# Kernel tuning notes

Hardware: AMD Instinct MI355X
Metric: run time of the kernel (lower is better)

## Reference

```python
import jax, jax.numpy as jnp
import numpy as np

NUM_CODES = 1024
EMBED_DIM = 64
COMMITMENT_COST = 0.25
ENTROPY_WEIGHT = 0.1
N_TOKENS = 131072


def setup_inputs() -> dict:
    key = jax.random.key(0)
    k1, k2 = jax.random.split(key)
    z_e = jax.random.normal(k1, (N_TOKENS, EMBED_DIM), dtype=jnp.float32)
    # nn.Embedding init: uniform(-1/num_codes, 1/num_codes)
    codebook = jax.random.uniform(
        k2, (NUM_CODES, EMBED_DIM), dtype=jnp.float32,
        minval=-1.0 / NUM_CODES, maxval=1.0 / NUM_CODES)
    return {"z_e": z_e, "codebook": codebook}


def reference(z_e, codebook):
    # Squared euclidean distances; argmin is invariant to sqrt so skip it.
    # d2[n,k] = |z_n|^2 - 2 z_n.e_k + |e_k|^2
    z_sq = jnp.sum(z_e * z_e, axis=-1, keepdims=True)          # [N,1]
    e_sq = jnp.sum(codebook * codebook, axis=-1)               # [K]
    d2 = z_sq - 2.0 * (z_e @ codebook.T) + e_sq[None, :]       # [N,K]
    indices = jnp.argmin(d2, axis=-1)                          # [N] int

    z_q = codebook[indices]                                    # [N,D] gather

    codebook_loss = jnp.mean((jax.lax.stop_gradient(z_q) - z_e) ** 2)
    commitment_loss = COMMITMENT_COST * jnp.mean(
        (z_q - jax.lax.stop_gradient(z_e)) ** 2)

    # Code-usage histogram via scatter-add (avoids materializing [N,K] one-hot).
    n = z_e.shape[0]
    counts = jnp.zeros((NUM_CODES,), dtype=z_e.dtype).at[indices].add(1.0)
    avg_probs = counts / n + 1e-10
    entropy = -jnp.sum(avg_probs * jnp.log(avg_probs))
    max_entropy = np.log(NUM_CODES)
    entropy_loss = -ENTROPY_WEIGHT * (entropy / max_entropy)
    perplexity = jnp.exp(entropy)

    # Straight-through estimator
    z_q_st = z_e + jax.lax.stop_gradient(z_q - z_e)

    return (z_q_st, indices, codebook_loss, commitment_loss,
            entropy_loss, perplexity)
```

## Files before the change

### kernel.cpp

```cpp
#include <hip/hip_runtime.h>
#include <float.h>
#include <math.h>

#define K_CODES 1024
#define ED 64
#define NTOK 131072
#define EPS 4e-4f

typedef __attribute__((ext_vector_type(8)))  short short8;
typedef __attribute__((ext_vector_type(16))) float float16;


static __device__ __forceinline__ unsigned short f2bf(float x) {
    unsigned u = __float_as_uint(x);
    u += 0x7fffu + ((u >> 16) & 1u);
    return (unsigned short)(u >> 16);
}
static __device__ __forceinline__ float bf2f(unsigned short h) {
    return __uint_as_float(((unsigned)h) << 16);
}

__global__ __launch_bounds__(256) void vq_codes(const float* __restrict__ cb,
                                                float* __restrict__ e_sq,
                                                short8* __restrict__ efH,
                                                short8* __restrict__ efL,
                                                unsigned int* __restrict__ counts,
                                                float* __restrict__ sse_part)
{
#pragma clang fp contract(off)
    const int k = blockIdx.x * 256 + threadIdx.x;
    const float4* ep = (const float4*)(cb + (size_t)k * ED);
    const int m = k & 31, ct = k >> 5;
    float r[8];
#pragma unroll
    for (int g = 0; g < 8; ++g) {
        float4 a = ep[2 * g], b = ep[2 * g + 1];
        float v[8] = {a.x, a.y, a.z, a.w, b.x, b.y, b.z, b.w};
        short8 hv, lv;
#pragma unroll
        for (int j = 0; j < 8; ++j) {
            unsigned short hb = f2bf(v[j]);
            hv[j] = (short)hb;
            lv[j] = (short)f2bf(v[j] - bf2f(hb));
            const float sq = v[j] * v[j];
            r[j] = g ? (r[j] + sq) : sq;
        }
        efH[(ct * 8 + g) * 32 + m] = hv;
        efL[(ct * 8 + g) * 32 + m] = lv;
    }
    e_sq[k] = ((r[0] + r[1]) + (r[2] + r[3])) + ((r[4] + r[5]) + (r[6] + r[7]));
    counts[k]        = 0u;
    counts[k + 1024] = 0u;
    counts[k + 2048] = 0u;
    counts[k + 3072] = 0u;
    if (k < 64) sse_part[k] = 0.f;
}

#define RESCORE(cc)                                                          \
    do {                                                                     \
        const int c_ = (cc);                                                 \
        const float4* e4_ = (const float4*)(cb + (size_t)c_ * ED);           \
        float a_ = 0.f;                                                      \
        _Pragma("unroll")                                                    \
        for (int jj_ = 0; jj_ < 16; ++jj_) {                                 \
            const float4 v_ = e4_[jj_];                                      \
            a_ = fmaf(zr[4 * jj_ + 0], v_.x, a_);                            \
            a_ = fmaf(zr[4 * jj_ + 1], v_.y, a_);                            \
            a_ = fmaf(zr[4 * jj_ + 2], v_.z, a_);                            \
            a_ = fmaf(zr[4 * jj_ + 3], v_.w, a_);                            \
        }                                                                    \
        const float d2_ = fmaf(-2.f, a_, zsq) + e_sq[c_];                    \
        if (d2_ < best || (d2_ == best && c_ < bi)) { best = d2_; bi = c_; } \
    } while (0)

__global__ __launch_bounds__(256, 3) void vq_main(const float* __restrict__ z_e,
                                                  const float* __restrict__ cb,
                                                  const float* __restrict__ e_sq,
                                                  const short8* __restrict__ efH,
                                                  const short8* __restrict__ efL,
                                                  float* __restrict__ out_zq,
                                                  float* __restrict__ out_idx,
                                                  unsigned int* __restrict__ counts,
                                                  float* __restrict__ sse_part)
{
#pragma clang fp contract(off)
    __shared__ short8 s_zfh[512];
    __shared__ short8 s_zfl[512];
    __shared__ float2 s_sel[32 * 64];
    __shared__ int    s_bi[64];
    __shared__ float  s_wsse[4];

    const int tid = threadIdx.x;
    const int wv = tid >> 6, lane = tid & 63;
    const int h = lane >> 5, ml = lane & 31;
    const int t0 = blockIdx.x * 64;

    {
        const float4* zp = (const float4*)(z_e + (size_t)(t0 + lane) * ED);
        const int n = lane & 31, ttl = lane >> 5;
#pragma unroll
        for (int gg = 0; gg < 2; ++gg) {
            const int g = wv * 2 + gg;
            float4 a = zp[2 * g], b = zp[2 * g + 1];
            float v[8] = {a.x, a.y, a.z, a.w, b.x, b.y, b.z, b.w};
            short8 hv, lv;
#pragma unroll
            for (int j = 0; j < 8; ++j) {
                unsigned short hb = f2bf(v[j]);
                hv[j] = (short)hb;
                lv[j] = (short)f2bf(v[j] - bf2f(hb));
            }
            s_zfh[(ttl * 8 + g) * 32 + n] = hv;
            s_zfl[(ttl * 8 + g) * 32 + n] = lv;
        }
    }
    __syncthreads();

#pragma unroll
    for (int g = 0; g < 4; ++g) {
        short8 ea[2][4], eb[2][4];
#pragma unroll
        for (int mt = 0; mt < 2; ++mt) {
            const int ct = g * 8 + wv * 2 + mt;
#pragma unroll
            for (int q = 0; q < 4; ++q) {
                const int idx = (ct * 8 + q * 2 + h) * 32 + ml;
                ea[mt][q] = efH[idx];
                eb[mt][q] = efL[idx];
            }
        }
#pragma unroll
        for (int it = 0; it < 2; ++it) {
            float16 acc0 = {}, acc1 = {};
#pragma unroll
            for (int q = 0; q < 4; ++q) {
                const int idx = (it * 8 + q * 2 + h) * 32 + ml;
                const short8 zh = s_zfh[idx];
                const short8 zl = s_zfl[idx];
                acc0 = __builtin_amdgcn_mfma_f32_32x32x16_bf16(ea[0][q], zh, acc0, 0, 0, 0);
                acc1 = __builtin_amdgcn_mfma_f32_32x32x16_bf16(ea[1][q], zh, acc1, 0, 0, 0);
                acc0 = __builtin_amdgcn_mfma_f32_32x32x16_bf16(ea[0][q], zl, acc0, 0, 0, 0);
                acc1 = __builtin_amdgcn_mfma_f32_32x32x16_bf16(ea[1][q], zl, acc1, 0, 0, 0);
                acc0 = __builtin_amdgcn_mfma_f32_32x32x16_bf16(eb[0][q], zh, acc0, 0, 0, 0);
                acc1 = __builtin_amdgcn_mfma_f32_32x32x16_bf16(eb[1][q], zh, acc1, 0, 0, 0);
            }
#pragma unroll
            for (int mt = 0; mt < 2; ++mt) {
                const float16 acc = mt ? acc1 : acc0;
                float tv1[8], tv2[8];
                int   ti[8];
#pragma unroll
                for (int p = 0; p < 8; ++p) {
                    const float a = acc[2 * p], b = acc[2 * p + 1];
                    const int ia = ((2 * p) & 3) + 8 * ((2 * p) >> 2) + 4 * h;
                    const int ib = ((2 * p + 1) & 3) + 8 * ((2 * p + 1) >> 2) + 4 * h;
                    const bool gt = b > a;
                    tv1[p] = gt ? b : a;
                    ti[p]  = gt ? ib : ia;
                    tv2[p] = gt ? a : b;
                }
#pragma unroll
                for (int s = 4; s >= 1; s >>= 1) {
#pragma unroll
                    for (int p = 0; p < s; ++p) {
                        const float av1 = tv1[2 * p], bv1 = tv1[2 * p + 1];
                        const bool gt = bv1 > av1;
                        const float inner = gt ? av1 : bv1;
                        tv1[p] = gt ? bv1 : av1;
                        ti[p]  = gt ? ti[2 * p + 1] : ti[2 * p];
                        tv2[p] = fmaxf(fmaxf(tv2[2 * p], tv2[2 * p + 1]), inner);
                    }
                }
                float v1 = tv1[0], v2 = tv2[0];
                int i1 = ti[0];
                const float o1 = __shfl_xor(v1, 32);
                const float o2 = __shfl_xor(v2, 32);
                const int   oi = __shfl_xor(i1, 32);
                const float lo = fminf(v1, o1);
                if (o1 > v1) { v1 = o1; i1 = oi; }
                v2 = fmaxf(lo, fmaxf(v2, o2));
                if (lane < 32) {
                    const unsigned bits = (__float_as_uint(-2.f * v1) & ~31u) | (unsigned)i1;
                    float2 o;
                    o.x = __uint_as_float(bits);
                    o.y = -2.f * v2;
                    s_sel[(g * 8 + wv * 2 + mt) * 64 + it * 32 + lane] = o;
                }
            }
        }
    }
    __syncthreads();

    if (wv < 2) {
        const int tls = (wv & 1) * 32 + ml;
        const int t = t0 + tls;
        float av[16], bv[16];
        float m = FLT_MAX;
#pragma unroll
        for (int i = 0; i < 16; ++i) {
            const float2 p = s_sel[(h * 16 + i) * 64 + tls];
            av[i] = p.x; bv[i] = p.y;
            m = fminf(m, av[i]);
        }
        m = fminf(m, __shfl_xor(m, 32));
        const float thr = m + EPS;

        unsigned band16 = 0u, full16 = 0u;
        int cand0 = 0, nb = 0;
#pragma unroll
        for (int i = 0; i < 16; ++i) {
            if (av[i] <= thr) {
                if (nb == 0)
                    cand0 = (h * 16 + i) * 32 + (int)(__float_as_uint(av[i]) & 31u);
                ++nb;
                band16 |= (1u << i);
                if (bv[i] <= thr) full16 |= (1u << i);
            }
        }
        const int nb_o = __shfl_xor(nb, 32);
        const int c0_o = __shfl_xor(cand0, 32);
        const unsigned full_o = (unsigned)__shfl_xor((int)full16, 32);

        int bsel;
        if ((nb + nb_o) == 1 && (full16 | full_o) == 0u) {
            bsel = h == 0 ? (nb ? cand0 : c0_o) : (nb_o ? c0_o : cand0);
        } else {
            const float4* zp = (const float4*)(z_e + (size_t)t * ED);
            float zr[ED];
#pragma unroll
            for (int i = 0; i < 16; ++i) {
                const float4 v = zp[i];
                zr[4 * i + 0] = v.x; zr[4 * i + 1] = v.y;
                zr[4 * i + 2] = v.z; zr[4 * i + 3] = v.w;
            }
            float r[8];
#pragma unroll
            for (int g2 = 0; g2 < 8; ++g2) {
#pragma unroll
                for (int j = 0; j < 8; ++j) {
                    const float sq = zr[g2 * 8 + j] * zr[g2 * 8 + j];
                    r[j] = g2 ? (r[j] + sq) : sq;
                }
            }
            const float zsq = ((r[0] + r[1]) + (r[2] + r[3])) + ((r[4] + r[5]) + (r[6] + r[7]));
            float best = FLT_MAX;
            int bi = 0;
            unsigned rem = band16;
            while (rem) {
                const int i = __ffs(rem) - 1;
                rem &= rem - 1;
                const int ct = h * 16 + i;
                if (full16 & (1u << i)) {
                    for (int j = 0; j < 32; ++j) RESCORE(ct * 32 + j);
                } else {
                    RESCORE(ct * 32 + (int)(__float_as_uint(av[i]) & 31u));
                }
            }
            const float ob  = __shfl_xor(best, 32);
            const int   obi = __shfl_xor(bi, 32);
            if (ob < best || (ob == best && obi < bi)) { best = ob; bi = obi; }
            bsel = bi;
        }

        if (h == 0) {
            s_bi[tls] = bsel;
            out_idx[t] = (float)bsel;
            atomicAdd(&counts[(blockIdx.x & 3) * K_CODES + bsel], 1u);
        }
    }
    __syncthreads();

    const float4* z4  = (const float4*)z_e + (size_t)t0 * 16;
    float4*       o4  = (float4*)out_zq + (size_t)t0 * 16;
    const float4* eq4 = (const float4*)cb;
    float lsse = 0.f;
#pragma unroll
    for (int p = 0; p < 4; ++p) {
        const int f = p * 256 + tid;
        const int bq = s_bi[f >> 4];
        const float4 q  = eq4[(size_t)bq * 16 + (f & 15)];
        const float4 zv = z4[f];
        o4[f] = q;
        float dx = q.x - zv.x; lsse = fmaf(dx, dx, lsse);
        float dy = q.y - zv.y; lsse = fmaf(dy, dy, lsse);
        float dz = q.z - zv.z; lsse = fmaf(dz, dz, lsse);
        float dw = q.w - zv.w; lsse = fmaf(dw, dw, lsse);
    }
#pragma unroll
    for (int off = 32; off > 0; off >>= 1)
        lsse += __shfl_down(lsse, off, 64);
    if (lane == 0) s_wsse[wv] = lsse;
    __syncthreads();
    if (tid == 0)
        atomicAdd(&sse_part[blockIdx.x & 63],
                  (s_wsse[0] + s_wsse[1]) + (s_wsse[2] + s_wsse[3]));
}

__global__ __launch_bounds__(1024) void vq_final(const unsigned int* __restrict__ counts,
                                                 const float* __restrict__ sse_part,
                                                 float* __restrict__ out_sc)
{
    __shared__ float red[1024];
    const int i = threadIdx.x;
    const unsigned int cu = counts[i] + counts[i + 1024]
                          + counts[i + 2048] + counts[i + 3072];
    const float c = (float)cu;
    const float p = c / (float)NTOK + 1e-10f;
    red[i] = p * logf(p);
    __syncthreads();
    for (int s = 512; s > 0; s >>= 1) {
        if (i < s) red[i] += red[i + s];
        __syncthreads();
    }
    if (i == 0) {
        const float entropy = -red[0];
        float ssum = 0.f;
        for (int k = 0; k < 64; ++k) ssum += sse_part[k];
        const float cbl = ssum / ((float)NTOK * (float)ED);
        out_sc[0] = cbl;
        out_sc[1] = 0.25f * cbl;
        out_sc[2] = -0.1f * (entropy / 6.93147180559945f);
        out_sc[3] = expf(entropy);
    }
}

extern "C" void kernel_launch(void* const* d_in, const int* in_sizes, int n_in,
                              void* d_out, int out_size, void* d_ws, size_t ws_size,
                              hipStream_t stream)
{
    const float* z_e = (const float*)d_in[0];
    const float* cb  = (const float*)d_in[1];

    float* out   = (float*)d_out;
    float* o_zq  = out;
    float* o_idx = out + (size_t)NTOK * ED;
    float* o_sc  = o_idx + NTOK;

    char* ws = (char*)d_ws;
    float*        e_sq     = (float*)(ws);
    unsigned int* counts   = (unsigned int*)(ws + 4096);
    float*        sse_part = (float*)(ws + 20480);
    short8*       efH      = (short8*)(ws + 32768);
    short8*       efL      = (short8*)(ws + 163840);

    vq_codes<<<4, 256, 0, stream>>>(cb, e_sq, efH, efL, counts, sse_part);
    vq_main <<<NTOK / 64, 256, 0, stream>>>(z_e, cb, e_sq, efH, efL,
                                            o_zq, o_idx, counts, sse_part);
    vq_final<<<1, 1024, 0, stream>>>(counts, sse_part, o_sc);
}
```

Before: 202.2 us.

## Spread candidate selection over all waves, prefetch z, fuse finalize via last-block

The candidate-selection and rescore phase now uses all four waves, with four lanes per token cooperating through xor shuffles, instead of only two waves with two lanes per token. The z tile for the SSE pass is loaded before the barrier so that its latency overlaps the selection work. The separate finalize kernel is removed: the last block to finish, found with an agent-scope atomic counter, computes entropy and the losses. The codebook prep kernel is split into 16 blocks of 64 threads. This trades one kernel launch for a fence and atomic per block plus extra registers held for the prefetched z.

```diff
diff --git a/kernel.cpp b/kernel.cpp
--- a/kernel.cpp
+++ b/kernel.cpp
@@ -20,15 +20,16 @@
     return __uint_as_float(((unsigned)h) << 16);
 }
 
-__global__ __launch_bounds__(256) void vq_codes(const float* __restrict__ cb,
-                                                float* __restrict__ e_sq,
-                                                short8* __restrict__ efH,
-                                                short8* __restrict__ efL,
-                                                unsigned int* __restrict__ counts,
-                                                float* __restrict__ sse_part)
+__global__ __launch_bounds__(64) void vq_codes(const float* __restrict__ cb,
+                                               float* __restrict__ e_sq,
+                                               short8* __restrict__ efH,
+                                               short8* __restrict__ efL,
+                                               unsigned int* __restrict__ counts,
+                                               float* __restrict__ sse_part,
+                                               unsigned int* __restrict__ done)
 {
 #pragma clang fp contract(off)
-    const int k = blockIdx.x * 256 + threadIdx.x;
+    const int k = blockIdx.x * 64 + threadIdx.x;
     const float4* ep = (const float4*)(cb + (size_t)k * ED);
     const int m = k & 31, ct = k >> 5;
     float r[8];
@@ -54,6 +55,7 @@
     counts[k + 2048] = 0u;
     counts[k + 3072] = 0u;
     if (k < 64) sse_part[k] = 0.f;
+    if (k == 0) *done = 0u;
 }
 
 #define RESCORE(cc)                                                          \
@@ -80,8 +82,10 @@
                                                   const short8* __restrict__ efL,
                                                   float* __restrict__ out_zq,
                                                   float* __restrict__ out_idx,
+                                                  float* __restrict__ out_sc,
                                                   unsigned int* __restrict__ counts,
-                                                  float* __restrict__ sse_part)
+                                                  float* __restrict__ sse_part,
+                                                  unsigned int* __restrict__ done)
 {
 #pragma clang fp contract(off)
     __shared__ short8 s_zfh[512];
@@ -89,6 +93,8 @@
     __shared__ float2 s_sel[32 * 64];
     __shared__ int    s_bi[64];
     __shared__ float  s_wsse[4];
+    __shared__ float  s_red[256];
+    __shared__ int    s_last;
 
     const int tid = threadIdx.x;
     const int wv = tid >> 6, lane = tid & 63;
@@ -189,41 +195,59 @@
             }
         }
     }
-    __syncthreads();
-
-    if (wv < 2) {
-        const int tls = (wv & 1) * 32 + ml;
+
+    const float4* z4  = (const float4*)z_e + (size_t)t0 * 16;
+    float4 zv[4];
+#pragma unroll
+    for (int p = 0; p < 4; ++p) zv[p] = z4[p * 256 + tid];
+    __syncthreads();
+
+    {
+        const int tls = tid >> 2;
+        const int sub = tid & 3;
         const int t = t0 + tls;
-        float av[16], bv[16];
+
+        float av[8], bv[8];
         float m = FLT_MAX;
 #pragma unroll
-        for (int i = 0; i < 16; ++i) {
-            const float2 p = s_sel[(h * 16 + i) * 64 + tls];
+        for (int i = 0; i < 8; ++i) {
+            const float2 p = s_sel[(sub * 8 + i) * 64 + tls];
             av[i] = p.x; bv[i] = p.y;
             m = fminf(m, av[i]);
         }
-        m = fminf(m, __shfl_xor(m, 32));
+        m = fminf(m, __shfl_xor(m, 1));
+        m = fminf(m, __shfl_xor(m, 2));
         const float thr = m + EPS;
 
-        unsigned band16 = 0u, full16 = 0u;
+        unsigned band8 = 0u, full8 = 0u;
         int cand0 = 0, nb = 0;
 #pragma unroll
-        for (int i = 0; i < 16; ++i) {
+        for (int i = 0; i < 8; ++i) {
             if (av[i] <= thr) {
                 if (nb == 0)
-                    cand0 = (h * 16 + i) * 32 + (int)(__float_as_uint(av[i]) & 31u);
+                    cand0 = (sub * 8 + i) * 32 + (int)(__float_as_uint(av[i]) & 31u);
                 ++nb;
-                band16 |= (1u << i);
-                if (bv[i] <= thr) full16 |= (1u << i);
-            }
-        }
-        const int nb_o = __shfl_xor(nb, 32);
-        const int c0_o = __shfl_xor(cand0, 32);
-        const unsigned full_o = (unsigned)__shfl_xor((int)full16, 32);
+                band8 |= (1u << i);
+                if (bv[i] <= thr) full8 |= (1u << i);
+            }
+        }
+        int fullany = (full8 != 0u);
+        {
+            int nb_o = __shfl_xor(nb, 1);
+            int c0_o = __shfl_xor(cand0, 1);
+            int fa_o = __shfl_xor(fullany, 1);
+            cand0 = ((sub & 1) == 0) ? (nb ? cand0 : c0_o) : (nb_o ? c0_o : cand0);
+            nb += nb_o; fullany |= fa_o;
+            nb_o = __shfl_xor(nb, 2);
+            c0_o = __shfl_xor(cand0, 2);
+            fa_o = __shfl_xor(fullany, 2);
+            cand0 = ((sub & 2) == 0) ? (nb ? cand0 : c0_o) : (nb_o ? c0_o : cand0);
+            nb += nb_o; fullany |= fa_o;
+        }
 
         int bsel;
-        if ((nb + nb_o) == 1 && (full16 | full_o) == 0u) {
-            bsel = h == 0 ? (nb ? cand0 : c0_o) : (nb_o ? c0_o : cand0);
+        if (nb == 1 && !fullany) {
+            bsel = cand0;
         } else {
             const float4* zp = (const float4*)(z_e + (size_t)t * ED);
             float zr[ED];
@@ -245,24 +269,27 @@
             const float zsq = ((r[0] + r[1]) + (r[2] + r[3])) + ((r[4] + r[5]) + (r[6] + r[7]));
             float best = FLT_MAX;
             int bi = 0;
-            unsigned rem = band16;
+            unsigned rem = band8;
             while (rem) {
                 const int i = __ffs(rem) - 1;
                 rem &= rem - 1;
-                const int ct = h * 16 + i;
-                if (full16 & (1u << i)) {
+                const int ct = sub * 8 + i;
+                if (full8 & (1u << i)) {
                     for (int j = 0; j < 32; ++j) RESCORE(ct * 32 + j);
                 } else {
                     RESCORE(ct * 32 + (int)(__float_as_uint(av[i]) & 31u));
                 }
             }
-            const float ob  = __shfl_xor(best, 32);
-            const int   obi = __shfl_xor(bi, 32);
-            if (ob < best || (ob == best && obi < bi)) { best = ob; bi = obi; }
+#pragma unroll
+            for (int d = 1; d <= 2; d <<= 1) {
+                const float ob  = __shfl_xor(best, d);
+                const int   obi = __shfl_xor(bi, d);
+                if (ob < best || (ob == best && obi < bi)) { best = ob; bi = obi; }
+            }
             bsel = bi;
         }
 
-        if (h == 0) {
+        if (sub == 0) {
             s_bi[tls] = bsel;
             out_idx[t] = (float)bsel;
             atomicAdd(&counts[(blockIdx.x & 3) * K_CODES + bsel], 1u);
@@ -270,21 +297,19 @@
     }
     __syncthreads();
 
-    const float4* z4  = (const float4*)z_e + (size_t)t0 * 16;
-    float4*       o4  = (float4*)out_zq + (size_t)t0 * 16;
+    float4* o4 = (float4*)out_zq + (size_t)t0 * 16;
     const float4* eq4 = (const float4*)cb;
     float lsse = 0.f;
 #pragma unroll
     for (int p = 0; p < 4; ++p) {
         const int f = p * 256 + tid;
         const int bq = s_bi[f >> 4];
-        const float4 q  = eq4[(size_t)bq * 16 + (f & 15)];
-        const float4 zv = z4[f];
+        const float4 q = eq4[(size_t)bq * 16 + (f & 15)];
         o4[f] = q;
-        float dx = q.x - zv.x; lsse = fmaf(dx, dx, lsse);
-        float dy = q.y - zv.y; lsse = fmaf(dy, dy, lsse);
-        float dz = q.z - zv.z; lsse = fmaf(dz, dz, lsse);
-        float dw = q.w - zv.w; lsse = fmaf(dw, dw, lsse);
+        float dx = q.x - zv[p].x; lsse = fmaf(dx, dx, lsse);
+        float dy = q.y - zv[p].y; lsse = fmaf(dy, dy, lsse);
+        float dz = q.z - zv[p].z; lsse = fmaf(dz, dz, lsse);
+        float dw = q.w - zv[p].w; lsse = fmaf(dw, dw, lsse);
     }
 #pragma unroll
     for (int off = 32; off > 0; off >>= 1)
@@ -294,33 +319,45 @@
     if (tid == 0)
         atomicAdd(&sse_part[blockIdx.x & 63],
                   (s_wsse[0] + s_wsse[1]) + (s_wsse[2] + s_wsse[3]));
-}
-
-__global__ __launch_bounds__(1024) void vq_final(const unsigned int* __restrict__ counts,
-                                                 const float* __restrict__ sse_part,
-                                                 float* __restrict__ out_sc)
-{
-    __shared__ float red[1024];
-    const int i = threadIdx.x;
-    const unsigned int cu = counts[i] + counts[i + 1024]
-                          + counts[i + 2048] + counts[i + 3072];
-    const float c = (float)cu;
-    const float p = c / (float)NTOK + 1e-10f;
-    red[i] = p * logf(p);
-    __syncthreads();
-    for (int s = 512; s > 0; s >>= 1) {
-        if (i < s) red[i] += red[i + s];
+
+    if (tid == 0) {
+        __threadfence();
+        const unsigned tk = __hip_atomic_fetch_add(done, 1u, __ATOMIC_ACQ_REL,
+                                                   __HIP_MEMORY_SCOPE_AGENT);
+        s_last = (tk == (unsigned)(gridDim.x - 1)) ? 1 : 0;
+    }
+    __syncthreads();
+    if (s_last) {
+        float part = 0.f;
+#pragma unroll
+        for (int j = 0; j < 4; ++j) {
+            const int i = tid + j * 256;
+            unsigned cu = 0;
+#pragma unroll
+            for (int sd = 0; sd < 4; ++sd)
+                cu += __hip_atomic_load(&counts[sd * K_CODES + i],
+                                        __ATOMIC_RELAXED, __HIP_MEMORY_SCOPE_AGENT);
+            const float p = (float)cu / (float)NTOK + 1e-10f;
+            part += p * logf(p);
+        }
+        s_red[tid] = part;
         __syncthreads();
-    }
-    if (i == 0) {
-        const float entropy = -red[0];
-        float ssum = 0.f;
-        for (int k = 0; k < 64; ++k) ssum += sse_part[k];
-        const float cbl = ssum / ((float)NTOK * (float)ED);
-        out_sc[0] = cbl;
-        out_sc[1] = 0.25f * cbl;
-        out_sc[2] = -0.1f * (entropy / 6.93147180559945f);
-        out_sc[3] = expf(entropy);
+        for (int s = 128; s > 0; s >>= 1) {
+            if (tid < s) s_red[tid] += s_red[tid + s];
+            __syncthreads();
+        }
+        if (tid == 0) {
+            const float entropy = -s_red[0];
+            float ssum = 0.f;
+            for (int k2 = 0; k2 < 64; ++k2)
+                ssum += __hip_atomic_load(&sse_part[k2],
+                                          __ATOMIC_RELAXED, __HIP_MEMORY_SCOPE_AGENT);
+            const float cbl = ssum / ((float)NTOK * (float)ED);
+            out_sc[0] = cbl;
+            out_sc[1] = 0.25f * cbl;
+            out_sc[2] = -0.1f * (entropy / 6.93147180559945f);
+            out_sc[3] = expf(entropy);
+        }
     }
 }
 
@@ -340,11 +377,12 @@
     float*        e_sq     = (float*)(ws);
     unsigned int* counts   = (unsigned int*)(ws + 4096);
     float*        sse_part = (float*)(ws + 20480);
+    unsigned int* done     = (unsigned int*)(ws + 20736);
     short8*       efH      = (short8*)(ws + 32768);
     short8*       efL      = (short8*)(ws + 163840);
 
-    vq_codes<<<4, 256, 0, stream>>>(cb, e_sq, efH, efL, counts, sse_part);
+    vq_codes<<<16, 64, 0, stream>>>(cb, e_sq, efH, efL, counts, sse_part, done);
     vq_main <<<NTOK / 64, 256, 0, stream>>>(z_e, cb, e_sq, efH, efL,
-                                            o_zq, o_idx, counts, sse_part);
-    vq_final<<<1, 1024, 0, stream>>>(counts, sse_part, o_sc);
-}
+                                            o_zq, o_idx, o_sc,
+                                            counts, sse_part, done);
+}
```

Result: slower. 258.2 us (+27.7%).
